# Kernel tuning notes

Measured on AMD Instinct MI355X. Metric: run time of the kernel, lower is better.

Reference implementation:

```python
import jax, jax.numpy as jnp
import numpy as np

B, S, HID = 2, 1024, 2048
H, HK, D = 32, 4, 128
G = H // HK
EPS = 1e-6
SCALE = 1.0 / np.sqrt(D)
ROPE_THETA = 1000000.0


def _rope_tables(seq_len, dim, theta):
    inv_freq = 1.0 / (theta ** (np.arange(0, dim, 2, dtype=np.float32) / dim))
    t = np.arange(seq_len, dtype=np.float32)
    freqs = np.outer(t, inv_freq)                      # [S, D/2]
    emb = np.concatenate([freqs, freqs], axis=-1)       # [S, D]
    return (jnp.asarray(np.cos(emb))[None, :, None, :],
            jnp.asarray(np.sin(emb))[None, :, None, :])  # [1,S,1,D]


def setup_inputs() -> dict:
    key = jax.random.key(0)
    k1, k2, k3 = jax.random.split(key, 3)
    cos, sin = _rope_tables(S, D, ROPE_THETA)
    return {
        "hidden_states": jax.random.normal(k1, (B, S, HID), jnp.float32),
        "cos": cos,
        "sin": sin,
        "w_qkv": jax.random.normal(k2, (HID, (H + 2 * HK) * D), jnp.float32) * 0.02,
        "q_norm_w": jnp.ones((D,), jnp.float32),
        "k_norm_w": jnp.ones((D,), jnp.float32),
        "w_o": jax.random.normal(k3, (H * D, HID), jnp.float32) * 0.02,
    }


def _rms_norm(x, w):
    xf = x.astype(jnp.float32)
    var = jnp.mean(xf * xf, axis=-1, keepdims=True)
    return (w * (xf * jax.lax.rsqrt(var + EPS))).astype(x.dtype)


def _rotate_half(x):
    x1, x2 = jnp.split(x, 2, axis=-1)
    return jnp.concatenate([-x2, x1], axis=-1)


def reference(hidden_states, cos, sin, w_qkv, q_norm_w, k_norm_w, w_o):
    b, s, _ = hidden_states.shape
    qkv = hidden_states @ w_qkv                          # [B,S,(H+2HK)*D]
    q, k, v = jnp.split(qkv, [H * D, (H + HK) * D], axis=-1)
    q = q.reshape(b, s, H, D)
    k = k.reshape(b, s, HK, D)
    v = v.reshape(b, s, HK, D)
    # per-head RMSNorm on q/k, then rotary (BSH layout)
    q = _rms_norm(q, q_norm_w)
    k = _rms_norm(k, k_norm_w)
    q = q * cos + _rotate_half(q) * sin
    k = k * cos + _rotate_half(k) * sin
    # grouped-query causal SDPA (prefill path, sparse_mode=2)
    qg = q.reshape(b, s, HK, G, D)
    scores = jnp.einsum("bqkgd,bskd->bkgqs", qg, k) * SCALE  # [B,HK,G,S,S]
    causal = jnp.tril(jnp.ones((s, s), bool))
    scores = jnp.where(causal, scores, jnp.finfo(scores.dtype).min)
    probs = jax.nn.softmax(scores, axis=-1)
    ctx = jnp.einsum("bkgqs,bskd->bqkgd", probs, v)          # [B,S,HK,G,D]
    ctx = ctx.reshape(b, s, H * D)
    return ctx @ w_o                                          # [B,S,HID]
```

## Files before the change

kernel.cpp:

```cpp
#include <hip/hip_runtime.h>

#define B_   2
#define S_   1024
#define HID_ 2048
#define H_   32
#define HK_  4
#define D_   128
#define NQKV ((H_ + 2 * HK_) * D_)
#define TOK  (B_ * S_)

typedef short bf16x8  __attribute__((ext_vector_type(8)));
typedef short short4v __attribute__((ext_vector_type(4)));
typedef float f32x4   __attribute__((ext_vector_type(4)));
typedef int   i32x4   __attribute__((ext_vector_type(4)));

__device__ inline short f2bf(float f) {
  unsigned u = __builtin_bit_cast(unsigned, f);
  u += 0x7fffu + ((u >> 16) & 1u);
  return (short)(u >> 16);
}
__device__ inline float bf2f(short s) {
  return __builtin_bit_cast(float, ((unsigned)(unsigned short)s) << 16);
}

__device__ __forceinline__ void gld_lds16(const short* g, short* l) {
  __builtin_amdgcn_global_load_lds((__attribute__((address_space(1))) void*)g,
                                   (__attribute__((address_space(3))) void*)l, 16, 0, 0);
}

__global__ __launch_bounds__(256) void cast_f32_bf16(const float* __restrict__ in,
                                                     short* __restrict__ out, int n4) {
  int i = blockIdx.x * 256 + threadIdx.x;
  if (i >= n4) return;
  f32x4 v = ((const f32x4*)in)[i];
  short4v o;
  o[0] = f2bf(v[0]); o[1] = f2bf(v[1]); o[2] = f2bf(v[2]); o[3] = f2bf(v[3]);
  ((short4v*)out)[i] = o;
}

__global__ __launch_bounds__(256) void transpose_cast(const float* __restrict__ in,
                                                      short* __restrict__ out,
                                                      int K, int N) {
  __shared__ float tile[32][33];
  int nb = blockIdx.x * 32, kb = blockIdx.y * 32;
  int c = threadIdx.x & 31, r0 = threadIdx.x >> 5;
#pragma unroll
  for (int i = 0; i < 4; i++) {
    int r = r0 + i * 8;
    tile[r][c] = in[(size_t)(kb + r) * N + nb + c];
  }
  __syncthreads();
#pragma unroll
  for (int i = 0; i < 4; i++) {
    int r = r0 + i * 8;
    out[(size_t)(nb + r) * K + kb + c] = f2bf(tile[c][r]);
  }
}

__global__ __launch_bounds__(256) void gemm_bt128(const short* __restrict__ A,
                                                  const short* __restrict__ Bt,
                                                  float* __restrict__ C,
                                                  int M, int N, int Kfull, int klen) {
  const int tid  = threadIdx.x;
  const int m0   = blockIdx.y * 128;
  const int n0   = blockIdx.x * 128;
  const int kz0  = blockIdx.z * klen;
  const int w    = tid >> 6, lane = tid & 63;
  const int quad = lane >> 4, l16 = lane & 15;
  const int wm   = (w >> 1) * 64, wn = (w & 1) * 64;

  __shared__ short As[128 * 64];
  __shared__ short Bs[128 * 64];

  const f32x4 z = {0.f, 0.f, 0.f, 0.f};
  f32x4 acc[4][4];
#pragma unroll
  for (int i = 0; i < 4; i++)
#pragma unroll
    for (int j = 0; j < 4; j++) acc[i][j] = z;

  const int srow = lane >> 3;
  const int lc   = (lane & 7) ^ srow;

  for (int kk = 0; kk < klen; kk += 64) {
    const int k0 = kz0 + kk;
#pragma unroll
    for (int i = 0; i < 4; i++) {
      int rb = w * 32 + i * 8;
      gld_lds16(&A [(size_t)(m0 + rb + srow) * Kfull + k0 + lc * 8], &As[rb * 64]);
      gld_lds16(&Bt[(size_t)(n0 + rb + srow) * Kfull + k0 + lc * 8], &Bs[rb * 64]);
    }
    __syncthreads();
#pragma unroll
    for (int kb = 0; kb < 2; kb++) {
      const int pc = ((kb * 4 + quad) ^ (l16 & 7)) * 8;
      bf16x8 a[4], b[4];
#pragma unroll
      for (int f = 0; f < 4; f++) {
        a[f] = *(const bf16x8*)&As[(wm + f * 16 + l16) * 64 + pc];
        b[f] = *(const bf16x8*)&Bs[(wn + f * 16 + l16) * 64 + pc];
      }
#pragma unroll
      for (int fi = 0; fi < 4; fi++)
#pragma unroll
        for (int fj = 0; fj < 4; fj++)
          acc[fi][fj] = __builtin_amdgcn_mfma_f32_16x16x32_bf16(a[fi], b[fj], acc[fi][fj], 0, 0, 0);
    }
    __syncthreads();
  }

  float* Cz = C + (size_t)blockIdx.z * M * N;
#pragma unroll
  for (int fi = 0; fi < 4; fi++) {
    int row0 = m0 + wm + fi * 16 + quad * 4;
#pragma unroll
    for (int fj = 0; fj < 4; fj++) {
      int col = n0 + wn + fj * 16 + l16;
#pragma unroll
      for (int r = 0; r < 4; r++)
        Cz[(size_t)(row0 + r) * N + col] = acc[fi][fj][r];
    }
  }
}

__global__ __launch_bounds__(256) void add2(const float* __restrict__ a,
                                            const float* __restrict__ b,
                                            float* __restrict__ c, int n4) {
  int i = blockIdx.x * 256 + threadIdx.x;
  if (i >= n4) return;
  f32x4 va = ((const f32x4*)a)[i], vb = ((const f32x4*)b)[i];
  ((f32x4*)c)[i] = va + vb;
}

__global__ __launch_bounds__(256) void gemm_qkv(const short* __restrict__ A,
                                                const short* __restrict__ Bt,
                                                const float* __restrict__ cosT,
                                                const float* __restrict__ sinT,
                                                const float* __restrict__ qw,
                                                const float* __restrict__ kw,
                                                short* __restrict__ Qb,
                                                short* __restrict__ Kb,
                                                short* __restrict__ Vt) {
  const int tid  = threadIdx.x;
  const int m0   = blockIdx.y * 128;
  const int n0   = blockIdx.x * 128;
  const int w    = tid >> 6, lane = tid & 63;
  const int quad = lane >> 4, l16 = lane & 15;
  const int wm   = (w >> 1) * 64, wn = (w & 1) * 64;

  __shared__ short As[128 * 64];
  __shared__ short Bs[128 * 64];
  __shared__ float ss_lds[4][64];

  const f32x4 z = {0.f, 0.f, 0.f, 0.f};
  f32x4 acc[4][4];
#pragma unroll
  for (int i = 0; i < 4; i++)
#pragma unroll
    for (int j = 0; j < 4; j++) acc[i][j] = z;

  const int srow = lane >> 3;
  const int lc   = (lane & 7) ^ srow;

  for (int k0 = 0; k0 < HID_; k0 += 64) {
#pragma unroll
    for (int i = 0; i < 4; i++) {
      int rb = w * 32 + i * 8;
      gld_lds16(&A [(size_t)(m0 + rb + srow) * HID_ + k0 + lc * 8], &As[rb * 64]);
      gld_lds16(&Bt[(size_t)(n0 + rb + srow) * HID_ + k0 + lc * 8], &Bs[rb * 64]);
    }
    __syncthreads();
#pragma unroll
    for (int kb = 0; kb < 2; kb++) {
      const int pc = ((kb * 4 + quad) ^ (l16 & 7)) * 8;
      bf16x8 a[4], b[4];
#pragma unroll
      for (int f = 0; f < 4; f++) {
        a[f] = *(const bf16x8*)&As[(wm + f * 16 + l16) * 64 + pc];
        b[f] = *(const bf16x8*)&Bs[(wn + f * 16 + l16) * 64 + pc];
      }
#pragma unroll
      for (int fi = 0; fi < 4; fi++)
#pragma unroll
        for (int fj = 0; fj < 4; fj++)
          acc[fi][fj] = __builtin_amdgcn_mfma_f32_16x16x32_bf16(a[fi], b[fj], acc[fi][fj], 0, 0, 0);
    }
    __syncthreads();
  }

  const int hd = n0 >> 7;
  const int bb = m0 >> 10;
  const int sW = (m0 & (S_ - 1)) + wm;

  if (hd >= H_ + HK_) {
    const int khv = hd - (H_ + HK_);
    short* dstV = Vt + ((size_t)(bb * HK_ + khv) * D_) * S_;
#pragma unroll
    for (int fi = 0; fi < 4; fi++) {
      int s = sW + fi * 16 + quad * 4;
#pragma unroll
      for (int fj = 0; fj < 4; fj++) {
        int d = wn + fj * 16 + l16;
        short4v o;
#pragma unroll
        for (int r = 0; r < 4; r++) o[r] = f2bf(acc[fi][fj][r]);
        *(short4v*)&dstV[(size_t)d * S_ + s] = o;
      }
    }
    return;
  }

  float ssp[4][4];
#pragma unroll
  for (int fi = 0; fi < 4; fi++)
#pragma unroll
    for (int r = 0; r < 4; r++) {
      float t = 0.f;
#pragma unroll
      for (int fj = 0; fj < 4; fj++) t += acc[fi][fj][r] * acc[fi][fj][r];
      ssp[fi][r] = t;
    }
#pragma unroll
  for (int off = 1; off < 16; off <<= 1)
#pragma unroll
    for (int fi = 0; fi < 4; fi++)
#pragma unroll
      for (int r = 0; r < 4; r++) ssp[fi][r] += __shfl_xor(ssp[fi][r], off, 64);
  if (l16 == 0)
#pragma unroll
    for (int fi = 0; fi < 4; fi++)
#pragma unroll
      for (int r = 0; r < 4; r++) ss_lds[w][fi * 16 + quad * 4 + r] = ssp[fi][r];
  __syncthreads();
  float rn[4][4];
#pragma unroll
  for (int fi = 0; fi < 4; fi++)
#pragma unroll
    for (int r = 0; r < 4; r++) {
      int row = fi * 16 + quad * 4 + r;
      rn[fi][r] = rsqrtf((ss_lds[w][row] + ss_lds[w ^ 1][row]) * (1.0f / 128.0f) + 1e-6f);
    }
  const float* wv = (hd < H_) ? qw : kw;
  float wgt[4];
#pragma unroll
  for (int fj = 0; fj < 4; fj++) wgt[fj] = wv[wn + fj * 16 + l16];

  short* xown = (w & 1) ? &Bs[(w >> 1) * 4096] : &As[(w >> 1) * 4096];
  short* xpar = (w & 1) ? &As[(w >> 1) * 4096] : &Bs[(w >> 1) * 4096];
#pragma unroll
  for (int fi = 0; fi < 4; fi++)
#pragma unroll
    for (int fj = 0; fj < 4; fj++) {
      short4v y4;
#pragma unroll
      for (int r = 0; r < 4; r++) y4[r] = f2bf(acc[fi][fj][r] * rn[fi][r] * wgt[fj]);
      *(short4v*)&xown[(((fi * 4 + fj) * 4 + quad) * 16 + l16) * 4] = y4;
    }
  __syncthreads();

  const float sign = (wn == 0) ? -1.0f : 1.0f;
  const float osc  = (hd < H_) ? (0.08838834764831845f * 1.4426950408889634f) : 1.0f;
  short* dstQ = (hd < H_) ? (Qb + (((size_t)bb * H_ + hd) * S_) * D_)
                          : (Kb + (((size_t)bb * HK_ + (hd - H_)) * S_) * D_);
#pragma unroll
  for (int fi = 0; fi < 4; fi++)
#pragma unroll
    for (int fj = 0; fj < 4; fj++) {
      short4v yp4 = *(const short4v*)&xpar[(((fi * 4 + fj) * 4 + quad) * 16 + l16) * 4];
      int d = wn + fj * 16 + l16;
#pragma unroll
      for (int r = 0; r < 4; r++) {
        int s = sW + fi * 16 + quad * 4 + r;
        float y  = acc[fi][fj][r] * rn[fi][r] * wgt[fj];
        float yp = bf2f(yp4[r]);
        float c  = cosT[s * D_ + d];
        float sn = sinT[s * D_ + d];
        dstQ[(size_t)s * D_ + d] = f2bf((y * c + sign * yp * sn) * osc);
      }
    }
}

__global__ __launch_bounds__(256) void attn_mfma5(const short* __restrict__ Qb,
                                                  const short* __restrict__ Kb,
                                                  const short* __restrict__ Vt,
                                                  short* __restrict__ ctx) {
  const int qmap[8] = {7, 0, 6, 1, 5, 2, 4, 3};
  const int qt = qmap[blockIdx.x & 7];
  const int h  = blockIdx.y;
  const int b  = blockIdx.z;
  const int kh = h >> 3;
  const int q0 = qt * 128;
  const int tid = threadIdx.x, w = tid >> 6, lane = tid & 63;
  const int quad = lane >> 4, l16 = lane & 15;
  const float MBIAS = 18.0f;

  __shared__ short Ks[128 * 64];
  __shared__ short Vs[144 * 64];
  __shared__ short Ps[4][2][16 * 72];

  for (int i = tid; i < 16 * 64; i += 256) Vs[128 * 64 + i] = (short)0x3F80;

  const short* Qbase = Qb + (((size_t)b * H_ + h) * S_ + q0) * D_;
  bf16x8 aq[2][4];
#pragma unroll
  for (int fi = 0; fi < 2; fi++)
#pragma unroll
    for (int kb = 0; kb < 4; kb++)
      aq[fi][kb] = *(const bf16x8*)&Qbase[(size_t)(fi * 64 + w * 16 + l16) * D_ + kb * 32 + quad * 8];

  const f32x4 z = {0.f, 0.f, 0.f, 0.f};
  f32x4 O[2][9];
#pragma unroll
  for (int fi = 0; fi < 2; fi++)
#pragma unroll
    for (int n = 0; n < 9; n++) O[fi][n] = z;

  const short* Kbase = Kb + ((size_t)(b * HK_ + kh) * S_) * D_;
  const short* Vbase = Vt + ((size_t)(b * HK_ + kh) * D_) * S_;

  const int srow = lane >> 3;
  const int lc   = (lane & 7) ^ srow;

  const int nkt = 2 * qt + 2;
  for (int kt = 0; kt < nkt; kt++) {
    const int k0 = kt * 64;
    __syncthreads();
#pragma unroll
    for (int i = 0; i < 4; i++) {
      int rb = w * 32 + i * 8;
      int rr = rb + srow;
      gld_lds16(&Kbase[(size_t)(k0 + (rr & 63)) * D_ + (rr >> 6) * 64 + lc * 8], &Ks[rb * 64]);
      gld_lds16(&Vbase[(size_t)rr * S_ + k0 + lc * 8], &Vs[rb * 64]);
    }
    __syncthreads();

#pragma unroll
    for (int nb = 0; nb < 4; nb++) {
      f32x4 s0 = z, s1 = z;
#pragma unroll
      for (int kb = 0; kb < 4; kb++) {
        const int c  = kb * 4 + quad;
        const int c7 = c & 7;
        const int rr = (c >> 3) * 64 + nb * 16 + l16;
        bf16x8 bk = *(const bf16x8*)&Ks[rr * 64 + (c7 ^ (l16 & 7)) * 8];
        s0 = __builtin_amdgcn_mfma_f32_16x16x32_bf16(aq[0][kb], bk, s0, 0, 0, 0);
        s1 = __builtin_amdgcn_mfma_f32_16x16x32_bf16(aq[1][kb], bk, s1, 0, 0, 0);
      }
      const int col = k0 + nb * 16 + l16;
#pragma unroll
      for (int r = 0; r < 4; r++) {
        int row0 = q0 + w * 16 + quad * 4 + r;
        float p0 = (col > row0) ? 0.0f : exp2f(s0[r] - MBIAS);
        float p1 = (col > row0 + 64) ? 0.0f : exp2f(s1[r] - MBIAS);
        Ps[w][0][(quad * 4 + r) * 72 + nb * 16 + l16] = f2bf(p0);
        Ps[w][1][(quad * 4 + r) * 72 + nb * 16 + l16] = f2bf(p1);
      }
    }

#pragma unroll
    for (int kb2 = 0; kb2 < 2; kb2++) {
      bf16x8 ap0 = *(const bf16x8*)&Ps[w][0][l16 * 72 + kb2 * 32 + quad * 8];
      bf16x8 ap1 = *(const bf16x8*)&Ps[w][1][l16 * 72 + kb2 * 32 + quad * 8];
      const int c7 = kb2 * 4 + quad;
#pragma unroll
      for (int nb2 = 0; nb2 < 9; nb2++) {
        int d = nb2 * 16 + l16;
        bf16x8 bv = *(const bf16x8*)&Vs[d * 64 + (c7 ^ (d & 7)) * 8];
        O[0][nb2] = __builtin_amdgcn_mfma_f32_16x16x32_bf16(ap0, bv, O[0][nb2], 0, 0, 0);
        O[1][nb2] = __builtin_amdgcn_mfma_f32_16x16x32_bf16(ap1, bv, O[1][nb2], 0, 0, 0);
      }
    }
  }

#pragma unroll
  for (int fi = 0; fi < 2; fi++)
#pragma unroll
    for (int r = 0; r < 4; r++) {
      float inv = 1.0f / O[fi][8][r];
      size_t row = (size_t)(b * S_ + q0 + fi * 64 + w * 16 + quad * 4 + r);
      short* dst = ctx + row * (H_ * D_) + h * D_;
#pragma unroll
      for (int nb2 = 0; nb2 < 8; nb2++)
        dst[nb2 * 16 + l16] = f2bf(O[fi][nb2][r] * inv);
    }
}

extern "C" void kernel_launch(void* const* d_in, const int* in_sizes, int n_in,
                              void* d_out, int out_size, void* d_ws, size_t ws_size,
                              hipStream_t stream) {
  (void)in_sizes; (void)n_in; (void)out_size; (void)ws_size;
  const float* hidden = (const float*)d_in[0];
  const float* cosT   = (const float*)d_in[1];
  const float* sinT   = (const float*)d_in[2];
  const float* wqkv   = (const float*)d_in[3];
  const float* qnw    = (const float*)d_in[4];
  const float* knw    = (const float*)d_in[5];
  const float* wo     = (const float*)d_in[6];
  float* out = (float*)d_out;

  char* ws = (char*)d_ws;
  short* Qb  = (short*)ws;
  short* Kb  = (short*)(ws + 16777216);
  short* Vt  = (short*)(ws + 16777216 + 2097152);
  short* hb  = (short*)(ws + 41943040);
  short* wT  = (short*)(ws + 41943040 + 8388608);
  short* ctx = (short*)(ws + 41943040 + 8388608 + 20971520);
  float* part = (float*)ws;

  cast_f32_bf16<<<4096, 256, 0, stream>>>(hidden, hb, TOK * HID_ / 4);
  transpose_cast<<<dim3(NQKV / 32, HID_ / 32), 256, 0, stream>>>(wqkv, wT, HID_, NQKV);
  gemm_qkv<<<dim3(NQKV / 128, TOK / 128), 256, 0, stream>>>(hb, wT, cosT, sinT, qnw, knw, Qb, Kb, Vt);
  attn_mfma5<<<dim3(S_ / 128, H_, B_), 256, 0, stream>>>(Qb, Kb, Vt, ctx);
  transpose_cast<<<dim3(HID_ / 32, (H_ * D_) / 32), 256, 0, stream>>>(wo, wT, H_ * D_, HID_);
  gemm_bt128<<<dim3(HID_ / 128, TOK / 128, 2), 256, 0, stream>>>(ctx, wT, part, TOK, HID_, H_ * D_, (H_ * D_) / 2);
  add2<<<(TOK * HID_ / 4 + 255) / 256, 256, 0, stream>>>(part, part + (size_t)TOK * HID_, out, TOK * HID_ / 4);
}
```

Before: 334.6 us.

## Use 256x256 double-buffered pipelined tile for fused QKV GEMM

Replaces the 128x128 single-buffered QKV GEMM with a 256x256 tile over 512 threads. It double-buffers LDS and interleaves global-to-LDS prefetch of the next K slices with MFMA phases, using barriers and wave priority hints. The RMSNorm/RoPE epilogue is adapted so each wave pair covers one head's 128 columns. The aim is more data reuse per load and latency hiding, at the risk of fewer blocks (160) than CUs and larger LDS use.

```diff
diff --git a/kernel.cpp b/kernel.cpp
--- a/kernel.cpp
+++ b/kernel.cpp
@@ -132,75 +132,148 @@
   ((f32x4*)c)[i] = va + vb;
 }
 
-__global__ __launch_bounds__(256) void gemm_qkv(const short* __restrict__ A,
-                                                const short* __restrict__ Bt,
-                                                const float* __restrict__ cosT,
-                                                const float* __restrict__ sinT,
-                                                const float* __restrict__ qw,
-                                                const float* __restrict__ kw,
-                                                short* __restrict__ Qb,
-                                                short* __restrict__ Kb,
-                                                short* __restrict__ Vt) {
+#define NT_ (HID_ / 64)
+
+__global__ __launch_bounds__(512, 2) void gemm_qkv256(const short* __restrict__ A,
+                                                      const short* __restrict__ Bt,
+                                                      const float* __restrict__ cosT,
+                                                      const float* __restrict__ sinT,
+                                                      const float* __restrict__ qw,
+                                                      const float* __restrict__ kw,
+                                                      short* __restrict__ Qb,
+                                                      short* __restrict__ Kb,
+                                                      short* __restrict__ Vt) {
   const int tid  = threadIdx.x;
-  const int m0   = blockIdx.y * 128;
-  const int n0   = blockIdx.x * 128;
+  const int m0   = blockIdx.y * 256;
+  const int n0   = blockIdx.x * 256;
   const int w    = tid >> 6, lane = tid & 63;
   const int quad = lane >> 4, l16 = lane & 15;
-  const int wm   = (w >> 1) * 64, wn = (w & 1) * 64;
-
-  __shared__ short As[128 * 64];
-  __shared__ short Bs[128 * 64];
-  __shared__ float ss_lds[4][64];
+  const int wm   = (w >> 2) * 128;
+  const int wn   = (w & 3) * 64;
+
+  __shared__ short As[2][256 * 64];
+  __shared__ short Bs[2][256 * 64];
 
   const f32x4 z = {0.f, 0.f, 0.f, 0.f};
-  f32x4 acc[4][4];
-#pragma unroll
-  for (int i = 0; i < 4; i++)
+  f32x4 acc[8][4];
+#pragma unroll
+  for (int i = 0; i < 8; i++)
 #pragma unroll
     for (int j = 0; j < 4; j++) acc[i][j] = z;
 
   const int srow = lane >> 3;
   const int lc   = (lane & 7) ^ srow;
-
-  for (int k0 = 0; k0 < HID_; k0 += 64) {
-#pragma unroll
-    for (int i = 0; i < 4; i++) {
-      int rb = w * 32 + i * 8;
-      gld_lds16(&A [(size_t)(m0 + rb + srow) * HID_ + k0 + lc * 8], &As[rb * 64]);
-      gld_lds16(&Bt[(size_t)(n0 + rb + srow) * HID_ + k0 + lc * 8], &Bs[rb * 64]);
-    }
-    __syncthreads();
-#pragma unroll
-    for (int kb = 0; kb < 2; kb++) {
-      const int pc = ((kb * 4 + quad) ^ (l16 & 7)) * 8;
-      bf16x8 a[4], b[4];
-#pragma unroll
-      for (int f = 0; f < 4; f++) {
-        a[f] = *(const bf16x8*)&As[(wm + f * 16 + l16) * 64 + pc];
-        b[f] = *(const bf16x8*)&Bs[(wn + f * 16 + l16) * 64 + pc];
-      }
-#pragma unroll
-      for (int fi = 0; fi < 4; fi++)
-#pragma unroll
-        for (int fj = 0; fj < 4; fj++)
-          acc[fi][fj] = __builtin_amdgcn_mfma_f32_16x16x32_bf16(a[fi], b[fj], acc[fi][fj], 0, 0, 0);
-    }
-    __syncthreads();
-  }
-
-  const int hd = n0 >> 7;
-  const int bb = m0 >> 10;
-  const int sW = (m0 & (S_ - 1)) + wm;
-
-  if (hd >= H_ + HK_) {
-    const int khv = hd - (H_ + HK_);
-    short* dstV = Vt + ((size_t)(bb * HK_ + khv) * D_) * S_;
-#pragma unroll
-    for (int fi = 0; fi < 4; fi++) {
+  const int rb   = w * 32;
+  const short* Ag = A  + (size_t)(m0 + rb + srow) * HID_ + lc * 8;
+  const short* Bg = Bt + (size_t)(n0 + rb + srow) * HID_ + lc * 8;
+
+#define STAGE_A(t_, c2_) do {                                                     \
+    short* dstA_ = &As[(t_) & 1][0]; const int k0A_ = (t_) * 64;                  \
+    gld_lds16(Ag + (size_t)((c2_) * 16    ) * HID_ + k0A_, dstA_ + (rb + (c2_) * 16    ) * 64); \
+    gld_lds16(Ag + (size_t)((c2_) * 16 + 8) * HID_ + k0A_, dstA_ + (rb + (c2_) * 16 + 8) * 64); \
+  } while (0)
+#define STAGE_B(t_, c2_) do {                                                     \
+    short* dstB_ = &Bs[(t_) & 1][0]; const int k0B_ = (t_) * 64;                  \
+    gld_lds16(Bg + (size_t)((c2_) * 16    ) * HID_ + k0B_, dstB_ + (rb + (c2_) * 16    ) * 64); \
+    gld_lds16(Bg + (size_t)((c2_) * 16 + 8) * HID_ + k0B_, dstB_ + (rb + (c2_) * 16 + 8) * 64); \
+  } while (0)
+
+  STAGE_A(0, 0); STAGE_A(0, 1); STAGE_B(0, 0); STAGE_B(0, 1);
+  STAGE_A(1, 0); STAGE_A(1, 1);
+  asm volatile("s_waitcnt vmcnt(4)" ::: "memory");
+  __builtin_amdgcn_s_barrier();
+  __builtin_amdgcn_sched_barrier(0);
+
+  for (int t = 0; t < NT_; ++t) {
+    const short* Ac = &As[t & 1][0];
+    const short* Bc = &Bs[t & 1][0];
+    bf16x8 bfr[4][2], a0[4][2], a1[4][2];
+
+#pragma unroll
+    for (int fj = 0; fj < 4; fj++)
+#pragma unroll
+      for (int kb = 0; kb < 2; kb++)
+        bfr[fj][kb] = *(const bf16x8*)&Bc[(wn + fj * 16 + l16) * 64 + (((kb * 4 + quad) ^ (l16 & 7)) * 8)];
+#pragma unroll
+    for (int fi = 0; fi < 4; fi++)
+#pragma unroll
+      for (int kb = 0; kb < 2; kb++)
+        a0[fi][kb] = *(const bf16x8*)&Ac[(wm + fi * 16 + l16) * 64 + (((kb * 4 + quad) ^ (l16 & 7)) * 8)];
+    if (t + 1 < NT_) STAGE_B(t + 1, 0);
+    __builtin_amdgcn_s_barrier();
+    __builtin_amdgcn_s_setprio(1);
+#pragma unroll
+    for (int fi = 0; fi < 4; fi++)
+#pragma unroll
+      for (int fj = 0; fj < 2; fj++)
+#pragma unroll
+        for (int kb = 0; kb < 2; kb++)
+          acc[fi][fj] = __builtin_amdgcn_mfma_f32_16x16x32_bf16(a0[fi][kb], bfr[fj][kb], acc[fi][fj], 0, 0, 0);
+    __builtin_amdgcn_s_setprio(0);
+
+#pragma unroll
+    for (int fi = 0; fi < 4; fi++)
+#pragma unroll
+      for (int kb = 0; kb < 2; kb++)
+        a1[fi][kb] = *(const bf16x8*)&Ac[(wm + 64 + fi * 16 + l16) * 64 + (((kb * 4 + quad) ^ (l16 & 7)) * 8)];
+    if (t + 1 < NT_) STAGE_B(t + 1, 1);
+    __builtin_amdgcn_s_barrier();
+    __builtin_amdgcn_s_setprio(1);
+#pragma unroll
+    for (int fi = 0; fi < 4; fi++)
+#pragma unroll
+      for (int fj = 2; fj < 4; fj++)
+#pragma unroll
+        for (int kb = 0; kb < 2; kb++)
+          acc[fi][fj] = __builtin_amdgcn_mfma_f32_16x16x32_bf16(a0[fi][kb], bfr[fj][kb], acc[fi][fj], 0, 0, 0);
+    __builtin_amdgcn_s_setprio(0);
+    asm volatile("s_waitcnt lgkmcnt(0)" ::: "memory");
+    __builtin_amdgcn_s_barrier();
+
+    if (t + 2 < NT_) STAGE_A(t + 2, 0);
+    __builtin_amdgcn_s_setprio(1);
+#pragma unroll
+    for (int fi = 0; fi < 4; fi++)
+#pragma unroll
+      for (int fj = 0; fj < 2; fj++)
+#pragma unroll
+        for (int kb = 0; kb < 2; kb++)
+          acc[4 + fi][fj] = __builtin_amdgcn_mfma_f32_16x16x32_bf16(a1[fi][kb], bfr[fj][kb], acc[4 + fi][fj], 0, 0, 0);
+    __builtin_amdgcn_s_setprio(0);
+
+    if (t + 2 < NT_) STAGE_A(t + 2, 1);
+    __builtin_amdgcn_s_setprio(1);
+#pragma unroll
+    for (int fi = 0; fi < 4; fi++)
+#pragma unroll
+      for (int fj = 2; fj < 4; fj++)
+#pragma unroll
+        for (int kb = 0; kb < 2; kb++)
+          acc[4 + fi][fj] = __builtin_amdgcn_mfma_f32_16x16x32_bf16(a1[fi][kb], bfr[fj][kb], acc[4 + fi][fj], 0, 0, 0);
+    __builtin_amdgcn_s_setprio(0);
+    if (t + 2 < NT_) { asm volatile("s_waitcnt vmcnt(4)" ::: "memory"); }
+    else             { asm volatile("s_waitcnt vmcnt(0)" ::: "memory"); }
+    __builtin_amdgcn_s_barrier();
+    __builtin_amdgcn_sched_barrier(0);
+  }
+#undef STAGE_A
+#undef STAGE_B
+
+  const int hd0 = n0 >> 7;
+  const int hs  = hd0 + ((w & 3) >> 1);
+  const int dh64 = (w & 1) * 64;
+  const int bb  = m0 >> 10;
+  const int sW  = (m0 & (S_ - 1)) + wm;
+
+  if (hd0 >= H_ + HK_) {
+    const int khv = hs - (H_ + HK_);
+    short* dstV = Vt + ((size_t)(bb * HK_ + khv) * D_ + dh64) * S_;
+#pragma unroll
+    for (int fi = 0; fi < 8; fi++) {
       int s = sW + fi * 16 + quad * 4;
 #pragma unroll
       for (int fj = 0; fj < 4; fj++) {
-        int d = wn + fj * 16 + l16;
+        int d = fj * 16 + l16;
         short4v o;
 #pragma unroll
         for (int r = 0; r < 4; r++) o[r] = f2bf(acc[fi][fj][r]);
@@ -210,45 +283,48 @@
     return;
   }
 
-  float ssp[4][4];
-#pragma unroll
-  for (int fi = 0; fi < 4; fi++)
+  float ssp[8][4];
+#pragma unroll
+  for (int fi = 0; fi < 8; fi++)
 #pragma unroll
     for (int r = 0; r < 4; r++) {
-      float t = 0.f;
-#pragma unroll
-      for (int fj = 0; fj < 4; fj++) t += acc[fi][fj][r] * acc[fi][fj][r];
-      ssp[fi][r] = t;
+      float tacc = 0.f;
+#pragma unroll
+      for (int fj = 0; fj < 4; fj++) tacc += acc[fi][fj][r] * acc[fi][fj][r];
+      ssp[fi][r] = tacc;
     }
 #pragma unroll
   for (int off = 1; off < 16; off <<= 1)
 #pragma unroll
-    for (int fi = 0; fi < 4; fi++)
+    for (int fi = 0; fi < 8; fi++)
 #pragma unroll
       for (int r = 0; r < 4; r++) ssp[fi][r] += __shfl_xor(ssp[fi][r], off, 64);
+
+  float* ss = (float*)&As[0][0];
   if (l16 == 0)
 #pragma unroll
-    for (int fi = 0; fi < 4; fi++)
-#pragma unroll
-      for (int r = 0; r < 4; r++) ss_lds[w][fi * 16 + quad * 4 + r] = ssp[fi][r];
+    for (int fi = 0; fi < 8; fi++)
+#pragma unroll
+      for (int r = 0; r < 4; r++) ss[w * 128 + fi * 16 + quad * 4 + r] = ssp[fi][r];
   __syncthreads();
-  float rn[4][4];
-#pragma unroll
-  for (int fi = 0; fi < 4; fi++)
+  float rn[8][4];
+#pragma unroll
+  for (int fi = 0; fi < 8; fi++)
 #pragma unroll
     for (int r = 0; r < 4; r++) {
       int row = fi * 16 + quad * 4 + r;
-      rn[fi][r] = rsqrtf((ss_lds[w][row] + ss_lds[w ^ 1][row]) * (1.0f / 128.0f) + 1e-6f);
-    }
-  const float* wv = (hd < H_) ? qw : kw;
+      rn[fi][r] = rsqrtf((ss[w * 128 + row] + ss[(w ^ 1) * 128 + row]) * (1.0f / 128.0f) + 1e-6f);
+    }
+  const float* wv = (hs < H_) ? qw : kw;
   float wgt[4];
 #pragma unroll
-  for (int fj = 0; fj < 4; fj++) wgt[fj] = wv[wn + fj * 16 + l16];
-
-  short* xown = (w & 1) ? &Bs[(w >> 1) * 4096] : &As[(w >> 1) * 4096];
-  short* xpar = (w & 1) ? &As[(w >> 1) * 4096] : &Bs[(w >> 1) * 4096];
-#pragma unroll
-  for (int fi = 0; fi < 4; fi++)
+  for (int fj = 0; fj < 4; fj++) wgt[fj] = wv[dh64 + fj * 16 + l16];
+  __syncthreads();
+
+  short* xown = ((w & 1) ? &Bs[0][0] : &As[0][0]) + (w >> 1) * 8192;
+  short* xpar = ((w & 1) ? &As[0][0] : &Bs[0][0]) + (w >> 1) * 8192;
+#pragma unroll
+  for (int fi = 0; fi < 8; fi++)
 #pragma unroll
     for (int fj = 0; fj < 4; fj++) {
       short4v y4;
@@ -258,16 +334,16 @@
     }
   __syncthreads();
 
-  const float sign = (wn == 0) ? -1.0f : 1.0f;
-  const float osc  = (hd < H_) ? (0.08838834764831845f * 1.4426950408889634f) : 1.0f;
-  short* dstQ = (hd < H_) ? (Qb + (((size_t)bb * H_ + hd) * S_) * D_)
-                          : (Kb + (((size_t)bb * HK_ + (hd - H_)) * S_) * D_);
-#pragma unroll
-  for (int fi = 0; fi < 4; fi++)
+  const float sign = (w & 1) ? 1.0f : -1.0f;
+  const float osc  = (hs < H_) ? (0.08838834764831845f * 1.4426950408889634f) : 1.0f;
+  short* dstQ = (hs < H_) ? (Qb + (((size_t)bb * H_ + hs) * S_) * D_)
+                          : (Kb + (((size_t)bb * HK_ + (hs - H_)) * S_) * D_);
+#pragma unroll
+  for (int fi = 0; fi < 8; fi++)
 #pragma unroll
     for (int fj = 0; fj < 4; fj++) {
       short4v yp4 = *(const short4v*)&xpar[(((fi * 4 + fj) * 4 + quad) * 16 + l16) * 4];
-      int d = wn + fj * 16 + l16;
+      int d = dh64 + fj * 16 + l16;
 #pragma unroll
       for (int r = 0; r < 4; r++) {
         int s = sW + fi * 16 + quad * 4 + r;
@@ -409,7 +485,7 @@
 
   cast_f32_bf16<<<4096, 256, 0, stream>>>(hidden, hb, TOK * HID_ / 4);
   transpose_cast<<<dim3(NQKV / 32, HID_ / 32), 256, 0, stream>>>(wqkv, wT, HID_, NQKV);
-  gemm_qkv<<<dim3(NQKV / 128, TOK / 128), 256, 0, stream>>>(hb, wT, cosT, sinT, qnw, knw, Qb, Kb, Vt);
+  gemm_qkv256<<<dim3(NQKV / 256, TOK / 256), 512, 0, stream>>>(hb, wT, cosT, sinT, qnw, knw, Qb, Kb, Vt);
   attn_mfma5<<<dim3(S_ / 128, H_, B_), 256, 0, stream>>>(Qb, Kb, Vt, ctx);
   transpose_cast<<<dim3(HID_ / 32, (H_ * D_) / 32), 256, 0, stream>>>(wo, wT, H_ * D_, HID_);
   gemm_bt128<<<dim3(HID_ / 128, TOK / 128, 2), 256, 0, stream>>>(ctx, wT, part, TOK, HID_, H_ * D_, (H_ * D_) / 2);
```

After: 338.1 us. No clear change (+1.1%).
